# Performance work log

Hardware: AMD Instinct MI355X
Metric: run time of the kernel (lower is better)

Reference implementation:

```python
import jax, jax.numpy as jnp
import numpy as np
from jax import lax

# Model dimensions (from init_kwargs)
I_SIZE, H_SIZE, O_SIZE = 256, 512, 256
N_NEURONS = I_SIZE + H_SIZE + O_SIZE   # 1024
N_ACTIVE = H_SIZE + O_SIZE             # 768 neurons in range(I_SIZE, N_NEURONS)
N_DIMS = 64
D_FEAT = 128


def _sphere(k, shape):
    # geoopt.Sphere().projx == L2 normalization of rows
    v = jax.random.normal(k, shape, dtype=jnp.float32)
    return v / jnp.linalg.norm(v, axis=-1, keepdims=True)


def setup_inputs() -> dict:
    key = jax.random.key(0)
    k0, k1, k2, k3, k4 = jax.random.split(key, 5)
    return {
        "x": jax.random.normal(k0, (I_SIZE, D_FEAT), dtype=jnp.float32),          # x[i] for input index i
        "pos_head": _sphere(k1, (N_NEURONS, N_DIMS)),
        "pos_tail": _sphere(k2, (N_NEURONS, N_DIMS)),
        "W": jax.random.normal(k3, (N_ACTIVE, D_FEAT, D_FEAT), dtype=jnp.float32) / np.float32(np.sqrt(D_FEAT)),
        "a": jax.random.normal(k4, (N_ACTIVE, N_NEURONS), dtype=jnp.float32),
    }


def reference(x, pos_head, pos_tail, W, a):
    # add_to_state: data_pos = tail positions of input indices 0..I_SIZE-1
    data_pos = pos_tail[:I_SIZE]                      # [i, n_dims]
    # _score: data_pos @ heads.T
    scores = data_pos @ pos_head.T                    # [i, n_neurons]
    # tau is identity per the source (self.tau = [lambda x: x ...]), so scores unchanged.
    # _aggregate: einsum('ij,kl->lj', data, scores) -> [n_neurons, d_feat]
    agg = jnp.einsum('ij,kl->lj', x, scores)
    # Per-neuron sequential transform loop over active indices range(I_SIZE, N_NEURONS):
    #   data = transforms[idx](data[order]);  transform_i(v) = tanh(outer(a_i, v @ W_i))
    orders = jnp.arange(N_ACTIVE)

    def step(carry, inp):
        Wt, at, t = inp
        v = carry[t]                                  # gather row `order` [d_feat]
        new = jnp.tanh(jnp.outer(at, v @ Wt))         # [n_neurons, d_feat]
        return new, new

    _, outs = lax.scan(step, agg, (W, a, orders))     # [n_active, n_neurons, d_feat]
    # First O_SIZE active indices lie in the output range [I_SIZE, I_SIZE+O_SIZE):
    # those iterations populate `out`; later (hidden) iterations only update state.
    return outs[:O_SIZE]                              # [o_size, n_neurons, d_feat]
```

## Files before the change

kernel.cpp:

```cpp
#include <hip/hip_runtime.h>
#include <math.h>

#define D_FEAT   128
#define O_SIZE   256
#define N_NEUR   1024
#define STEPS_PER_WG 4
#define N_WG     (O_SIZE / STEPS_PER_WG)

typedef unsigned long long ull;
typedef float floatx4 __attribute__((ext_vector_type(4)));

__device__ __align__(16) float g_u[O_SIZE * D_FEAT];
__device__ ull g_chan[N_WG][D_FEAT];

#define TAG_INVALID 0xFFFFFFFFu

__device__ __forceinline__ float tanh_fast(float x) {
    x = fminf(fmaxf(x, -20.f), 20.f);
    float e = __expf(2.f * x);
    return (e - 1.f) * __builtin_amdgcn_rcpf(e + 1.f);
}

__global__ __launch_bounds__(1024) void init_kernel(
    const float* __restrict__ x,
    const float* __restrict__ pos_head,
    const float* __restrict__ pos_tail)
{
    __shared__ float psum[8][D_FEAT];
    __shared__ float ptps[8][64];
    __shared__ float red[64];

    const int tid = threadIdx.x;

    for (int i = tid; i < (N_WG - 1) * D_FEAT; i += 1024)
        g_chan[1 + i / D_FEAT][i % D_FEAT] = ((ull)TAG_INVALID) << 32;

    {
        const int s = tid >> 7, j = tid & 127;
        float acc = 0.f;
        #pragma unroll 8
        for (int ii = 0; ii < 32; ++ii)
            acc += x[(s * 32 + ii) * D_FEAT + j];
        psum[s][j] = acc;
    }
    if (tid < 512) {
        const int kb = tid >> 6, d = tid & 63;
        float acc = 0.f;
        #pragma unroll 8
        for (int kk = 0; kk < 32; ++kk)
            acc += pos_tail[(kb * 32 + kk) * 64 + d];
        ptps[kb][d] = acc;
    }
    __syncthreads();

    if (tid < 64) {
        float ptd = 0.f;
        #pragma unroll
        for (int kb = 0; kb < 8; ++kb) ptd += ptps[kb][tid];
        red[tid] = ptd * pos_head[tid];
    }
    __syncthreads();

    if (tid < 128) {
        float sx = 0.f;
        #pragma unroll
        for (int s = 0; s < 8; ++s) sx += psum[s][tid];
        float ss0 = 0.f;
        #pragma unroll
        for (int d = 0; d < 64; ++d) ss0 += red[d];
        const float v0 = ss0 * sx;
        g_chan[0][tid] =  (ull)__float_as_uint(v0);
    }
}

__global__ __launch_bounds__(1024) void chain_kernel(
    const float* __restrict__ W,
    const float* __restrict__ a)
{
    __shared__ float v_lds[D_FEAT];
    __shared__ float psum[8][D_FEAT];

    const int bid = blockIdx.x;
    const int g   = ((bid & 7) << 3) | (bid >> 3);
    const int tid = threadIdx.x;
    const int s   = tid >> 7;
    const int j   = tid & 127;
    const int t0  = g * STEPS_PER_WG;

    float w[STEPS_PER_WG][16];
    #pragma unroll
    for (int k = 0; k < STEPS_PER_WG; ++k) {
        #pragma unroll
        for (int m = 0; m < 16; ++m)
            w[k][m] = W[((size_t)(t0 + k) * D_FEAT + (s * 16 + m)) * D_FEAT + j];
    }
    float ascal[STEPS_PER_WG];
    #pragma unroll
    for (int k = 0; k < STEPS_PER_WG; ++k)
        ascal[k] = a[(t0 + k) * N_NEUR + (t0 + k) + 1];

    float dummy = 0.f;
    #pragma unroll
    for (int k = 0; k < STEPS_PER_WG; ++k) {
        #pragma unroll
        for (int m = 0; m < 16; ++m) {
            asm volatile("" : "+v"(w[k][m]));
            dummy += w[k][m];
        }
        asm volatile("" : "+v"(ascal[k]));
    }
    asm volatile("" :: "v"(dummy));

    if (tid < 128) {
        ull pk;
        for (;;) {
            pk = __hip_atomic_load(&g_chan[g][j], __ATOMIC_RELAXED,
                                   __HIP_MEMORY_SCOPE_AGENT);
            if ((unsigned)(pk >> 32) == (unsigned)g) break;
            __builtin_amdgcn_s_sleep(1);
        }
        v_lds[j] = __uint_as_float((unsigned)pk);
    }
    __syncthreads();

    #pragma unroll
    for (int k = 0; k < STEPS_PER_WG; ++k) {
        const int t = t0 + k;
        float acc = 0.f;
        #pragma unroll
        for (int m = 0; m < 16; ++m)
            acc += v_lds[s * 16 + m] * w[k][m];
        psum[s][j] = acc;
        __syncthreads();

        if (tid < 128) {
            float u = 0.f;
            #pragma unroll
            for (int ss = 0; ss < 8; ++ss) u += psum[ss][j];
            g_u[t * D_FEAT + j] = u;
            const float vn = tanh_fast(ascal[k] * u);
            if (k < STEPS_PER_WG - 1) {
                v_lds[j] = vn;
            } else if (g + 1 < N_WG) {
                const ull pk = (((ull)(unsigned)(g + 1)) << 32) |
                               (ull)__float_as_uint(vn);
                __hip_atomic_store(&g_chan[g + 1][j], pk, __ATOMIC_RELAXED,
                                   __HIP_MEMORY_SCOPE_AGENT);
            }
        }
        __syncthreads();
    }
}

__global__ __launch_bounds__(256) void out_kernel(
    const float* __restrict__ a,
    float* __restrict__ out)
{
    const long gid = (long)blockIdx.x * 256 + threadIdx.x;
    const long row = gid >> 5;
    const int  jq  = (int)(gid & 31);
    const int  t   = (int)(row >> 10);

    const float   s  = a[row];
    const floatx4 u4 = ((const floatx4*)g_u)[t * 32 + jq];

    floatx4 r;
    r.x = tanh_fast(s * u4.x);
    r.y = tanh_fast(s * u4.y);
    r.z = tanh_fast(s * u4.z);
    r.w = tanh_fast(s * u4.w);

    __builtin_nontemporal_store(r, (floatx4*)out + row * 32 + jq);
}

extern "C" void kernel_launch(void* const* d_in, const int* in_sizes, int n_in,
                              void* d_out, int out_size, void* d_ws, size_t ws_size,
                              hipStream_t stream)
{
    const float* x        = (const float*)d_in[0];
    const float* pos_head = (const float*)d_in[1];
    const float* pos_tail = (const float*)d_in[2];
    const float* W        = (const float*)d_in[3];
    const float* a        = (const float*)d_in[4];
    float*       out      = (float*)d_out;

    hipLaunchKernelGGL(init_kernel, dim3(1), dim3(1024), 0, stream,
                       x, pos_head, pos_tail);

    hipLaunchKernelGGL(chain_kernel, dim3(N_WG), dim3(1024), 0, stream,
                       W, a);

    hipLaunchKernelGGL(out_kernel, dim3(32768), dim3(256), 0, stream,
                       a, out);
}
```

Before: 316.8 us.

## Fuse init, chain and output into one persistent kernel with streaming writers

```diff
diff --git a/kernel.cpp b/kernel.cpp
--- a/kernel.cpp
+++ b/kernel.cpp
@@ -5,15 +5,19 @@
 #define O_SIZE   256
 #define N_NEUR   1024
 #define STEPS_PER_WG 4
-#define N_WG     (O_SIZE / STEPS_PER_WG)
+#define N_CHAIN_WG   (O_SIZE / STEPS_PER_WG)
+#define N_WRITER_WG  192
+#define N_BLOCKS     (N_CHAIN_WG + N_WRITER_WG)
+#define N_ITEMS      (O_SIZE * 8)
 
 typedef unsigned long long ull;
 typedef float floatx4 __attribute__((ext_vector_type(4)));
 
-__device__ __align__(16) float g_u[O_SIZE * D_FEAT];
-__device__ ull g_chan[N_WG][D_FEAT];
-
-#define TAG_INVALID 0xFFFFFFFFu
+__device__ ull      g_chan[N_CHAIN_WG][D_FEAT];
+__device__ ull      g_uchan[O_SIZE][D_FEAT];
+__device__ unsigned g_uflag[O_SIZE];
+__device__ unsigned g_gen  = 1u;
+__device__ int      g_done = 0;
 
 __device__ __forceinline__ float tanh_fast(float x) {
     x = fminf(fmaxf(x, -20.f), 20.f);
@@ -21,156 +25,180 @@
     return (e - 1.f) * __builtin_amdgcn_rcpf(e + 1.f);
 }
 
-__global__ __launch_bounds__(1024) void init_kernel(
+__global__ __launch_bounds__(1024) void fused_kernel(
     const float* __restrict__ x,
     const float* __restrict__ pos_head,
-    const float* __restrict__ pos_tail)
-{
-    __shared__ float psum[8][D_FEAT];
-    __shared__ float ptps[8][64];
-    __shared__ float red[64];
-
-    const int tid = threadIdx.x;
-
-    for (int i = tid; i < (N_WG - 1) * D_FEAT; i += 1024)
-        g_chan[1 + i / D_FEAT][i % D_FEAT] = ((ull)TAG_INVALID) << 32;
-
-    {
-        const int s = tid >> 7, j = tid & 127;
-        float acc = 0.f;
-        #pragma unroll 8
-        for (int ii = 0; ii < 32; ++ii)
-            acc += x[(s * 32 + ii) * D_FEAT + j];
-        psum[s][j] = acc;
-    }
-    if (tid < 512) {
-        const int kb = tid >> 6, d = tid & 63;
-        float acc = 0.f;
-        #pragma unroll 8
-        for (int kk = 0; kk < 32; ++kk)
-            acc += pos_tail[(kb * 32 + kk) * 64 + d];
-        ptps[kb][d] = acc;
-    }
-    __syncthreads();
-
-    if (tid < 64) {
-        float ptd = 0.f;
-        #pragma unroll
-        for (int kb = 0; kb < 8; ++kb) ptd += ptps[kb][tid];
-        red[tid] = ptd * pos_head[tid];
-    }
-    __syncthreads();
-
-    if (tid < 128) {
-        float sx = 0.f;
-        #pragma unroll
-        for (int s = 0; s < 8; ++s) sx += psum[s][tid];
-        float ss0 = 0.f;
-        #pragma unroll
-        for (int d = 0; d < 64; ++d) ss0 += red[d];
-        const float v0 = ss0 * sx;
-        g_chan[0][tid] =  (ull)__float_as_uint(v0);
-    }
-}
-
-__global__ __launch_bounds__(1024) void chain_kernel(
+    const float* __restrict__ pos_tail,
     const float* __restrict__ W,
-    const float* __restrict__ a)
-{
-    __shared__ float v_lds[D_FEAT];
-    __shared__ float psum[8][D_FEAT];
-
-    const int bid = blockIdx.x;
-    const int g   = ((bid & 7) << 3) | (bid >> 3);
-    const int tid = threadIdx.x;
-    const int s   = tid >> 7;
-    const int j   = tid & 127;
-    const int t0  = g * STEPS_PER_WG;
-
-    float w[STEPS_PER_WG][16];
-    #pragma unroll
-    for (int k = 0; k < STEPS_PER_WG; ++k) {
-        #pragma unroll
-        for (int m = 0; m < 16; ++m)
-            w[k][m] = W[((size_t)(t0 + k) * D_FEAT + (s * 16 + m)) * D_FEAT + j];
-    }
-    float ascal[STEPS_PER_WG];
-    #pragma unroll
-    for (int k = 0; k < STEPS_PER_WG; ++k)
-        ascal[k] = a[(t0 + k) * N_NEUR + (t0 + k) + 1];
-
-    float dummy = 0.f;
-    #pragma unroll
-    for (int k = 0; k < STEPS_PER_WG; ++k) {
-        #pragma unroll
-        for (int m = 0; m < 16; ++m) {
-            asm volatile("" : "+v"(w[k][m]));
-            dummy += w[k][m];
-        }
-        asm volatile("" : "+v"(ascal[k]));
-    }
-    asm volatile("" :: "v"(dummy));
-
-    if (tid < 128) {
-        ull pk;
-        for (;;) {
-            pk = __hip_atomic_load(&g_chan[g][j], __ATOMIC_RELAXED,
-                                   __HIP_MEMORY_SCOPE_AGENT);
-            if ((unsigned)(pk >> 32) == (unsigned)g) break;
-            __builtin_amdgcn_s_sleep(1);
-        }
-        v_lds[j] = __uint_as_float((unsigned)pk);
-    }
-    __syncthreads();
-
-    #pragma unroll
-    for (int k = 0; k < STEPS_PER_WG; ++k) {
-        const int t = t0 + k;
-        float acc = 0.f;
-        #pragma unroll
-        for (int m = 0; m < 16; ++m)
-            acc += v_lds[s * 16 + m] * w[k][m];
-        psum[s][j] = acc;
-        __syncthreads();
-
-        if (tid < 128) {
-            float u = 0.f;
-            #pragma unroll
-            for (int ss = 0; ss < 8; ++ss) u += psum[ss][j];
-            g_u[t * D_FEAT + j] = u;
-            const float vn = tanh_fast(ascal[k] * u);
-            if (k < STEPS_PER_WG - 1) {
-                v_lds[j] = vn;
-            } else if (g + 1 < N_WG) {
-                const ull pk = (((ull)(unsigned)(g + 1)) << 32) |
-                               (ull)__float_as_uint(vn);
-                __hip_atomic_store(&g_chan[g + 1][j], pk, __ATOMIC_RELAXED,
-                                   __HIP_MEMORY_SCOPE_AGENT);
-            }
-        }
-        __syncthreads();
-    }
-}
-
-__global__ __launch_bounds__(256) void out_kernel(
     const float* __restrict__ a,
     float* __restrict__ out)
 {
-    const long gid = (long)blockIdx.x * 256 + threadIdx.x;
-    const long row = gid >> 5;
-    const int  jq  = (int)(gid & 31);
-    const int  t   = (int)(row >> 10);
-
-    const float   s  = a[row];
-    const floatx4 u4 = ((const floatx4*)g_u)[t * 32 + jq];
-
-    floatx4 r;
-    r.x = tanh_fast(s * u4.x);
-    r.y = tanh_fast(s * u4.y);
-    r.z = tanh_fast(s * u4.z);
-    r.w = tanh_fast(s * u4.w);
-
-    __builtin_nontemporal_store(r, (floatx4*)out + row * 32 + jq);
+    const int bid = blockIdx.x;
+    const int tid = threadIdx.x;
+    const unsigned gen = g_gen;
+
+    if (bid < N_CHAIN_WG) {
+        __shared__ float v_lds[D_FEAT];
+        __shared__ float psum[8][D_FEAT];
+        __shared__ float ptps[8][64];
+        __shared__ float red[64];
+
+        const int g  = ((bid & 7) << 3) | (bid >> 3);
+        const int s  = tid >> 7;
+        const int j  = tid & 127;
+        const int t0 = g * STEPS_PER_WG;
+
+        float w[STEPS_PER_WG][16];
+        #pragma unroll
+        for (int k = 0; k < STEPS_PER_WG; ++k) {
+            #pragma unroll
+            for (int m = 0; m < 16; ++m)
+                w[k][m] = W[((size_t)(t0 + k) * D_FEAT + (s * 16 + m)) * D_FEAT + j];
+        }
+        float ascal[STEPS_PER_WG];
+        #pragma unroll
+        for (int k = 0; k < STEPS_PER_WG; ++k)
+            ascal[k] = a[(t0 + k) * N_NEUR + (t0 + k) + 1];
+
+        if (g == 0) {
+            {
+                float acc = 0.f;
+                #pragma unroll 8
+                for (int ii = 0; ii < 32; ++ii)
+                    acc += x[(s * 32 + ii) * D_FEAT + j];
+                psum[s][j] = acc;
+            }
+            if (tid < 512) {
+                const int kb = tid >> 6, d = tid & 63;
+                float acc = 0.f;
+                #pragma unroll 8
+                for (int kk = 0; kk < 32; ++kk)
+                    acc += pos_tail[(kb * 32 + kk) * 64 + d];
+                ptps[kb][d] = acc;
+            }
+            __syncthreads();
+            if (tid < 64) {
+                float ptd = 0.f;
+                #pragma unroll
+                for (int kb = 0; kb < 8; ++kb) ptd += ptps[kb][tid];
+                red[tid] = ptd * pos_head[tid];
+            }
+            __syncthreads();
+            if (tid < 128) {
+                float sx = 0.f;
+                #pragma unroll
+                for (int s8 = 0; s8 < 8; ++s8) sx += psum[s8][tid];
+                float ss0 = 0.f;
+                #pragma unroll
+                for (int d = 0; d < 64; ++d) ss0 += red[d];
+                v_lds[tid] = ss0 * sx;
+            }
+        }
+
+        float dummy = 0.f;
+        #pragma unroll
+        for (int k = 0; k < STEPS_PER_WG; ++k) {
+            #pragma unroll
+            for (int m = 0; m < 16; ++m) {
+                asm volatile("" : "+v"(w[k][m]));
+                dummy += w[k][m];
+            }
+            asm volatile("" : "+v"(ascal[k]));
+        }
+        asm volatile("" :: "v"(dummy));
+
+        if (g > 0 && tid < 128) {
+            const unsigned want = (gen << 8) | (unsigned)g;
+            ull pk;
+            for (;;) {
+                pk = __hip_atomic_load(&g_chan[g][j], __ATOMIC_RELAXED,
+                                       __HIP_MEMORY_SCOPE_AGENT);
+                if ((unsigned)(pk >> 32) == want) break;
+                __builtin_amdgcn_s_sleep(1);
+            }
+            v_lds[j] = __uint_as_float((unsigned)pk);
+        }
+        __syncthreads();
+
+        #pragma unroll
+        for (int k = 0; k < STEPS_PER_WG; ++k) {
+            const int t = t0 + k;
+            float acc = 0.f;
+            #pragma unroll
+            for (int m = 0; m < 16; ++m)
+                acc += v_lds[s * 16 + m] * w[k][m];
+            psum[s][j] = acc;
+            __syncthreads();
+
+            if (tid < 128) {
+                float u = 0.f;
+                #pragma unroll
+                for (int ss = 0; ss < 8; ++ss) u += psum[ss][j];
+                const ull upk = (((ull)((gen << 8) | (unsigned)t)) << 32) |
+                                (ull)__float_as_uint(u);
+                __hip_atomic_store(&g_uchan[t][j], upk, __ATOMIC_RELAXED,
+                                   __HIP_MEMORY_SCOPE_AGENT);
+                const float vn = tanh_fast(ascal[k] * u);
+                if (k < STEPS_PER_WG - 1) {
+                    v_lds[j] = vn;
+                } else if (g + 1 < N_CHAIN_WG) {
+                    const ull pk = (((ull)((gen << 8) | (unsigned)(g + 1))) << 32) |
+                                   (ull)__float_as_uint(vn);
+                    __hip_atomic_store(&g_chan[g + 1][j], pk, __ATOMIC_RELAXED,
+                                       __HIP_MEMORY_SCOPE_AGENT);
+                }
+            }
+            __syncthreads();
+            if (tid == 0)
+                __hip_atomic_store(&g_uflag[t], (gen << 8) | (unsigned)t,
+                                   __ATOMIC_RELEASE, __HIP_MEMORY_SCOPE_AGENT);
+        }
+    } else {
+        const int wid = bid - N_CHAIN_WG;
+        const int j4  = tid & 31;
+        for (int i = wid; i < N_ITEMS; i += N_WRITER_WG) {
+            const int t = i >> 3;
+            const int c = i & 7;
+            const unsigned want = (gen << 8) | (unsigned)t;
+            if (tid == 0) {
+                while (__hip_atomic_load(&g_uflag[t], __ATOMIC_RELAXED,
+                                         __HIP_MEMORY_SCOPE_AGENT) != want)
+                    __builtin_amdgcn_s_sleep(8);
+            }
+            __syncthreads();
+
+            const ull e0 = __hip_atomic_load(&g_uchan[t][4 * j4 + 0], __ATOMIC_RELAXED, __HIP_MEMORY_SCOPE_AGENT);
+            const ull e1 = __hip_atomic_load(&g_uchan[t][4 * j4 + 1], __ATOMIC_RELAXED, __HIP_MEMORY_SCOPE_AGENT);
+            const ull e2 = __hip_atomic_load(&g_uchan[t][4 * j4 + 2], __ATOMIC_RELAXED, __HIP_MEMORY_SCOPE_AGENT);
+            const ull e3 = __hip_atomic_load(&g_uchan[t][4 * j4 + 3], __ATOMIC_RELAXED, __HIP_MEMORY_SCOPE_AGENT);
+            const float u0 = __uint_as_float((unsigned)e0);
+            const float u1 = __uint_as_float((unsigned)e1);
+            const float u2 = __uint_as_float((unsigned)e2);
+            const float u3 = __uint_as_float((unsigned)e3);
+
+            const int lbase = (c << 7) + (tid >> 5);
+            #pragma unroll
+            for (int p = 0; p < 4; ++p) {
+                const int row = (t << 10) + lbase + (p << 5);
+                const float sc = a[row];
+                floatx4 r;
+                r.x = tanh_fast(sc * u0);
+                r.y = tanh_fast(sc * u1);
+                r.z = tanh_fast(sc * u2);
+                r.w = tanh_fast(sc * u3);
+                __builtin_nontemporal_store(r, (floatx4*)out + (((size_t)row) << 5) + j4);
+            }
+        }
+    }
+
+    __syncthreads();
+    if (tid == 0) {
+        const int old = atomicAdd(&g_done, 1);
+        if (old == N_BLOCKS - 1) {
+            __hip_atomic_store(&g_done, 0, __ATOMIC_RELAXED, __HIP_MEMORY_SCOPE_AGENT);
+            __hip_atomic_store(&g_gen, gen + 1u, __ATOMIC_RELAXED, __HIP_MEMORY_SCOPE_AGENT);
+        }
+    }
 }
 
 extern "C" void kernel_launch(void* const* d_in, const int* in_sizes, int n_in,
@@ -184,12 +212,6 @@
     const float* a        = (const float*)d_in[4];
     float*       out      = (float*)d_out;
 
-    hipLaunchKernelGGL(init_kernel, dim3(1), dim3(1024), 0, stream,
-                       x, pos_head, pos_tail);
-
-    hipLaunchKernelGGL(chain_kernel, dim3(N_WG), dim3(1024), 0, stream,
-                       W, a);
-
-    hipLaunchKernelGGL(out_kernel, dim3(32768), dim3(256), 0, stream,
-                       a, out);
+    hipLaunchKernelGGL(fused_kernel, dim3(N_BLOCKS), dim3(1024), 0, stream,
+                       x, pos_head, pos_tail, W, a, out);
 }
```

Result: slower. 366.0 us (+15.5%).
